# Kernel optimization log

Measured on AMD Instinct MI355X. Metric: run time of the kernel, lower is better.

Reference implementation:

```python
import jax, jax.numpy as jnp
import numpy as np
import math

HIDDEN = 1024
N_HEADS = 16
N_KV = 4
HEAD_DIM = HIDDEN // N_HEADS  # 64
B, S = 2, 2048
THETA = 100000.0


def _freqs_cos_sin(dim, end, theta):
    # yarn params: original_max_position_embeddings=2048 >= end, so no ramp scaling,
    # attention_factor=1.0 -> plain RoPE frequencies.
    inv = 1.0 / theta ** (np.arange(0, dim, 2)[: dim // 2] / dim)
    t = np.arange(end)
    f = np.outer(t, inv).astype(np.float32)  # (end, dim/2)
    cos = np.concatenate([np.cos(f), np.cos(f)], axis=-1)  # (end, dim)
    sin = np.concatenate([np.sin(f), np.sin(f)], axis=-1)
    return jnp.asarray(cos), jnp.asarray(sin)


def _rotate(x):
    # stack([-x[...,1::2], x[...,::2]], -1).reshape_as(x)
    return jnp.stack([-x[..., 1::2], x[..., ::2]], axis=-1).reshape(x.shape)


def setup_inputs() -> dict:
    key = jax.random.key(0)
    ks = jax.random.split(key, 9)
    s = 0.02
    return {
        "hidden_states": jax.random.normal(ks[0], (B, S, HIDDEN), jnp.float32),
        "attention_mask": jnp.ones((B, S), jnp.int32),
        "Wq": jax.random.normal(ks[1], (HIDDEN, HIDDEN), jnp.float32) * s,
        "bq": jnp.zeros((HIDDEN,), jnp.float32),
        "Wk": jax.random.normal(ks[2], (HIDDEN, N_KV * HEAD_DIM), jnp.float32) * s,
        "bk": jnp.zeros((N_KV * HEAD_DIM,), jnp.float32),
        "Wv": jax.random.normal(ks[3], (HIDDEN, N_KV * HEAD_DIM), jnp.float32) * s,
        "bv": jnp.zeros((N_KV * HEAD_DIM,), jnp.float32),
        "Wo": jax.random.normal(ks[4], (HIDDEN, HIDDEN), jnp.float32) * s,
        "bo": jnp.zeros((HIDDEN,), jnp.float32),
    }


def reference(hidden_states, attention_mask, Wq, bq, Wk, bk, Wv, bv, Wo, bo):
    b, s, _ = hidden_states.shape
    q = (hidden_states @ Wq + bq).reshape(b, s, N_HEADS, HEAD_DIM)
    k = (hidden_states @ Wk + bk).reshape(b, s, N_KV, HEAD_DIM)
    v = (hidden_states @ Wv + bv).reshape(b, s, N_KV, HEAD_DIM)

    cos, sin = _freqs_cos_sin(HEAD_DIM, s, THETA)
    cos = cos[:, None, :]  # (s,1,d) broadcasts over (b,s,h,d)
    sin = sin[:, None, :]
    q = q * cos + _rotate(q) * sin
    k = k * cos + _rotate(k) * sin

    # GQA: repeat_interleave kv heads -> jnp.repeat along head axis
    rep = N_HEADS // N_KV
    k = jnp.repeat(k, rep, axis=2)
    v = jnp.repeat(v, rep, axis=2)

    scores = jnp.einsum("bqhd,bkhd->bhqk", q, k) / math.sqrt(HEAD_DIM)
    neg = jnp.finfo(scores.dtype).min
    causal = jnp.triu(jnp.ones((s, s), bool), k=1)  # (q,kv)
    bias = jnp.where(causal, neg, 0.0).astype(scores.dtype)[None, None]
    key_mask = attention_mask.astype(bool)[:, None, None, :]  # (b,1,1,kv)
    bias = jnp.where(key_mask, bias, neg)
    probs = jax.nn.softmax(scores + bias, axis=-1)
    attn = jnp.einsum("bhqk,bkhd->bqhd", probs, v).reshape(b, s, HIDDEN)
    return attn @ Wo + bo
```

## Files before the change

kernel.cpp:

```cpp
#include <hip/hip_runtime.h>
#include <cstddef>
#include <cstdint>

#define B_   2
#define S_   2048
#define HID  1024
#define NH_  16
#define NKV_ 4
#define DH_  64
#define ROWS (B_ * S_)
#define NQKV 1536
#define QSCALE 0.18033688011112042f

typedef __bf16 bf16_t;
typedef _Float16 f16_t;
typedef bf16_t bf16x8 __attribute__((ext_vector_type(8)));
typedef bf16_t bf16x4 __attribute__((ext_vector_type(4)));
typedef f16_t  f16x8  __attribute__((ext_vector_type(8)));
typedef f16_t  f16x4  __attribute__((ext_vector_type(4)));
typedef float  f32x4  __attribute__((ext_vector_type(4)));

typedef __attribute__((address_space(1))) const uint32_t gu32_t;
typedef __attribute__((address_space(3))) uint32_t lu32_t;

__device__ __forceinline__ void gl_lds16(const void* g, void* l) {
  __builtin_amdgcn_global_load_lds((gu32_t*)g, (lu32_t*)l, 16, 0, 0);
}

__global__ void prep_all(const float* __restrict__ hs,
                         const float* __restrict__ Wq, const float* __restrict__ Wk,
                         const float* __restrict__ Wv, const float* __restrict__ Wo,
                         const float* __restrict__ bq, const float* __restrict__ bk,
                         const float* __restrict__ bv,
                         bf16_t* __restrict__ hsb,
                         bf16_t* __restrict__ Wt, bf16_t* __restrict__ Wot,
                         float* __restrict__ ball, float2* __restrict__ lut)
{
  const int bid = blockIdx.x;
  if (bid < 2048) {
    const int i = (bid * 256 + threadIdx.x) * 8;
    float4 a = *(const float4*)(hs + i);
    float4 b = *(const float4*)(hs + i + 4);
    bf16x8 o;
    o[0]=(bf16_t)a.x; o[1]=(bf16_t)a.y; o[2]=(bf16_t)a.z; o[3]=(bf16_t)a.w;
    o[4]=(bf16_t)b.x; o[5]=(bf16_t)b.y; o[6]=(bf16_t)b.z; o[7]=(bf16_t)b.w;
    *(bf16x8*)(hsb + i) = o;
    return;
  }
  if (bid >= 4614) {
    const int idx = (bid - 4614) * 256 + threadIdx.x;
    const int s = idx >> 5, j = idx & 31;
    const float L = 0.51905126482615037f;
    const float ang = (float)s * exp2f(-L * (float)j);
    lut[idx] = make_float2(cosf(ang), sinf(ang));
    return;
  }
  if (bid >= 4608) {
    int i = (bid - 4608) * 256 + threadIdx.x;
    if (i < NQKV) ball[i] = (i < 1024) ? bq[i] : ((i < 1280) ? bk[i-1024] : bv[i-1280]);
    return;
  }
  const int wb = bid - 2048;
  const float* src; bf16_t* dst; int N, n0, k0;
  if (wb < 1024)      { src = Wq; dst = Wt;            N = 1024; int t = wb;      n0=(t&31)*32; k0=(t>>5)*32; }
  else if (wb < 1280) { src = Wk; dst = Wt + 1024*HID; N = 256;  int t = wb-1024; n0=(t&7)*32;  k0=(t>>3)*32; }
  else if (wb < 1536) { src = Wv; dst = Wt + 1280*HID; N = 256;  int t = wb-1280; n0=(t&7)*32;  k0=(t>>3)*32; }
  else                { src = Wo; dst = Wot;           N = 1024; int t = wb-1536; n0=(t&31)*32; k0=(t>>5)*32; }
  __shared__ bf16_t T[32][33];
  const int tx = threadIdx.x & 31, ty = threadIdx.x >> 5;
#pragma unroll
  for (int i = 0; i < 4; ++i)
    T[ty + i*8][tx] = (bf16_t)src[(size_t)(k0 + ty + i*8) * N + n0 + tx];
  __syncthreads();
#pragma unroll
  for (int i = 0; i < 4; ++i)
    dst[(size_t)(n0 + ty + i*8) * HID + k0 + tx] = T[tx][ty + i*8];
}

__global__ __launch_bounds__(256, 3) void gemm_qkv(
    const bf16_t* __restrict__ A, const bf16_t* __restrict__ Bt,
    const float* __restrict__ bias, const float2* __restrict__ lut,
    bf16_t* __restrict__ C, bf16_t* __restrict__ Kimg, f16_t* __restrict__ Vimg)
{
  __shared__ bf16_t As[2][128 * 64];
  __shared__ bf16_t Bs[2][64 * 64];
  const int tid  = threadIdx.x;
  const int w    = tid >> 6;
  const int lane = tid & 63;
  const int m    = lane & 15;
  const int quad = lane >> 4;
  const int wm   = w >> 1, wn = w & 1;

  const int lin = blockIdx.y * 24 + blockIdx.x;
  const int swz = (lin & 7) * 96 + (lin >> 3);
  const int bx  = swz % 24;
  const int by  = swz / 24;
  const size_t bm = (size_t)by * 128;
  const size_t bn = (size_t)bx * 64;

  const int srow = w * 8 + (lane >> 3);
  const int scol = (lane & 7) * 8;
  const bf16_t* Ag = A  + (bm + srow) * HID + scol;
  const bf16_t* Bg = Bt + (bn + srow) * HID + scol;

  f32x4 acc[4][2];
#pragma unroll
  for (int i = 0; i < 4; ++i)
#pragma unroll
    for (int j = 0; j < 2; ++j) acc[i][j] = (f32x4){0.f, 0.f, 0.f, 0.f};

#pragma unroll
  for (int i = 0; i < 4; ++i)
    gl_lds16(Ag + (size_t)(i * 32) * HID, &As[0][(w * 8 + i * 32) * 64]);
#pragma unroll
  for (int i = 0; i < 2; ++i)
    gl_lds16(Bg + (size_t)(i * 32) * HID, &Bs[0][(w * 8 + i * 32) * 64]);

  int p = 0;
  for (int k0 = 0; k0 < HID; k0 += 64) {
    __syncthreads();
    if (k0 + 64 < HID) {
#pragma unroll
      for (int i = 0; i < 4; ++i)
        gl_lds16(Ag + (size_t)(i * 32) * HID + k0 + 64, &As[p^1][(w * 8 + i * 32) * 64]);
#pragma unroll
      for (int i = 0; i < 2; ++i)
        gl_lds16(Bg + (size_t)(i * 32) * HID + k0 + 64, &Bs[p^1][(w * 8 + i * 32) * 64]);
    }
#pragma unroll
    for (int ks = 0; ks < 2; ++ks) {
      bf16x8 af[4], bfr[2];
#pragma unroll
      for (int mt = 0; mt < 4; ++mt)
        af[mt] = *(const bf16x8*)&As[p][(wm * 64 + mt * 16 + m) * 64 + ks * 32 + quad * 8];
#pragma unroll
      for (int nt = 0; nt < 2; ++nt)
        bfr[nt] = *(const bf16x8*)&Bs[p][(wn * 32 + nt * 16 + m) * 64 + ks * 32 + quad * 8];
#pragma unroll
      for (int mt = 0; mt < 4; ++mt)
#pragma unroll
        for (int nt = 0; nt < 2; ++nt)
          acc[mt][nt] = __builtin_amdgcn_mfma_f32_16x16x32_bf16(bfr[nt], af[mt], acc[mt][nt], 0, 0, 0);
    }
    p ^= 1;
  }

  const int b   = by >> 4;
  const int rt  = by & 15;

  if (bx < 16) {
#pragma unroll
    for (int mt = 0; mt < 4; ++mt) {
      const size_t row = bm + wm * 64 + mt * 16 + m;
#pragma unroll
      for (int nt = 0; nt < 2; ++nt) {
        const size_t col = bn + wn * 32 + nt * 16 + quad * 4;
        float4 bb = *(const float4*)&bias[col];
        bf16x4 o;
        o[0] = (bf16_t)(acc[mt][nt][0] + bb.x);
        o[1] = (bf16_t)(acc[mt][nt][1] + bb.y);
        o[2] = (bf16_t)(acc[mt][nt][2] + bb.z);
        o[3] = (bf16_t)(acc[mt][nt][3] + bb.w);
        *(bf16x4*)&C[row * NQKV + col] = o;
      }
    }
  } else if (bx < 20) {
    const int kvh = bx - 16;
    const size_t img0 = ((size_t)(b * NKV_ + kvh) * 32 + rt * 2) * 4096;
#pragma unroll
    for (int mt = 0; mt < 4; ++mt) {
      const int row128 = wm * 64 + mt * 16 + m;
      const int srw    = rt * 128 + row128;
      const int key    = row128 & 63;
      const size_t img = img0 + (size_t)(row128 >> 6) * 4096;
#pragma unroll
      for (int nt = 0; nt < 2; ++nt) {
        const int d0 = wn * 32 + nt * 16 + quad * 4;
        const float4 bb = *(const float4*)&bias[1024 + kvh * DH_ + d0];
        const float v0 = acc[mt][nt][0] + bb.x;
        const float v1 = acc[mt][nt][1] + bb.y;
        const float v2 = acc[mt][nt][2] + bb.z;
        const float v3 = acc[mt][nt][3] + bb.w;
        const float2* lp = lut + srw * 32 + (d0 & 31);
        const float2 l0 = lp[0], l1 = lp[1], l2 = lp[2], l3 = lp[3];
        bf16x4 o;
        o[0] = (bf16_t)(v0 * l0.x - v1 * l0.y);
        o[1] = (bf16_t)(v1 * l1.x + v0 * l1.y);
        o[2] = (bf16_t)(v2 * l2.x - v3 * l2.y);
        o[3] = (bf16_t)(v3 * l3.x + v2 * l3.y);
        const int slot = (d0 >> 3) ^ (key & 7);
        *(bf16x4*)&Kimg[img + key * 64 + slot * 8 + (d0 & 7)] = o;
      }
    }
  } else {
    const int kvh = bx - 20;
    f16_t* Lv = (f16_t*)&As[0][0];
    __syncthreads();
#pragma unroll
    for (int mt = 0; mt < 4; ++mt) {
      const int row128 = wm * 64 + mt * 16 + m;
#pragma unroll
      for (int nt = 0; nt < 2; ++nt) {
        const int d0 = wn * 32 + nt * 16 + quad * 4;
        const float4 bb = *(const float4*)&bias[1280 + kvh * DH_ + d0];
        f16x4 o;
        o[0] = (f16_t)(acc[mt][nt][0] + bb.x);
        o[1] = (f16_t)(acc[mt][nt][1] + bb.y);
        o[2] = (f16_t)(acc[mt][nt][2] + bb.z);
        o[3] = (f16_t)(acc[mt][nt][3] + bb.w);
        *(f16x4*)&Lv[row128 * 68 + d0] = o;
      }
    }
    __syncthreads();
    const size_t img0 = ((size_t)(b * NKV_ + kvh) * 32 + rt * 2) * 4096;
    const int d  = tid & 63;
    const int qg = tid >> 6;
#pragma unroll
    for (int i = 0; i < 8; ++i) {
      const int ki = i >> 2;
      const int g4 = qg * 4 + (i & 3);
      f16x4 o;
#pragma unroll
      for (int j = 0; j < 4; ++j)
        o[j] = Lv[(ki * 64 + g4 * 4 + j) * 68 + d];
      const int slot = g4 ^ (d & 15);
      *(f16x4*)&Vimg[img0 + (size_t)ki * 4096 + d * 64 + slot * 4] = o;
    }
  }
}

__global__ __launch_bounds__(256, 3) void gemm64_f32o(
    const bf16_t* __restrict__ A, const bf16_t* __restrict__ Bt,
    const float* __restrict__ bias, float* __restrict__ C, int N)
{
  __shared__ bf16_t As[2][128 * 64];
  __shared__ bf16_t Bs[2][64 * 64];
  const int tid  = threadIdx.x;
  const int w    = tid >> 6;
  const int lane = tid & 63;
  const int m    = lane & 15;
  const int quad = lane >> 4;
  const int wm   = w >> 1, wn = w & 1;

  const int lin = blockIdx.y * 16 + blockIdx.x;
  const int swz = (lin & 7) * 64 + (lin >> 3);
  const int bx  = swz & 15;
  const int by  = swz >> 4;
  const size_t bm = (size_t)by * 128;
  const size_t bn = (size_t)bx * 64;

  const int srow = w * 8 + (lane >> 3);
  const int scol = (lane & 7) * 8;
  const bf16_t* Ag = A  + (bm + srow) * HID + scol;
  const bf16_t* Bg = Bt + (bn + srow) * HID + scol;

  f32x4 acc[4][2];
#pragma unroll
  for (int i = 0; i < 4; ++i)
#pragma unroll
    for (int j = 0; j < 2; ++j) acc[i][j] = (f32x4){0.f, 0.f, 0.f, 0.f};

#pragma unroll
  for (int i = 0; i < 4; ++i)
    gl_lds16(Ag + (size_t)(i * 32) * HID, &As[0][(w * 8 + i * 32) * 64]);
#pragma unroll
  for (int i = 0; i < 2; ++i)
    gl_lds16(Bg + (size_t)(i * 32) * HID, &Bs[0][(w * 8 + i * 32) * 64]);

  int p = 0;
  for (int k0 = 0; k0 < HID; k0 += 64) {
    __syncthreads();
    if (k0 + 64 < HID) {
#pragma unroll
      for (int i = 0; i < 4; ++i)
        gl_lds16(Ag + (size_t)(i * 32) * HID + k0 + 64, &As[p^1][(w * 8 + i * 32) * 64]);
#pragma unroll
      for (int i = 0; i < 2; ++i)
        gl_lds16(Bg + (size_t)(i * 32) * HID + k0 + 64, &Bs[p^1][(w * 8 + i * 32) * 64]);
    }
#pragma unroll
    for (int ks = 0; ks < 2; ++ks) {
      bf16x8 af[4], bfr[2];
#pragma unroll
      for (int mt = 0; mt < 4; ++mt)
        af[mt] = *(const bf16x8*)&As[p][(wm * 64 + mt * 16 + m) * 64 + ks * 32 + quad * 8];
#pragma unroll
      for (int nt = 0; nt < 2; ++nt)
        bfr[nt] = *(const bf16x8*)&Bs[p][(wn * 32 + nt * 16 + m) * 64 + ks * 32 + quad * 8];
#pragma unroll
      for (int mt = 0; mt < 4; ++mt)
#pragma unroll
        for (int nt = 0; nt < 2; ++nt)
          acc[mt][nt] = __builtin_amdgcn_mfma_f32_16x16x32_bf16(bfr[nt], af[mt], acc[mt][nt], 0, 0, 0);
    }
    p ^= 1;
  }
#pragma unroll
  for (int mt = 0; mt < 4; ++mt) {
    const size_t row = bm + wm * 64 + mt * 16 + m;
#pragma unroll
    for (int nt = 0; nt < 2; ++nt) {
      const size_t col = bn + wn * 32 + nt * 16 + quad * 4;
      float4 bb = *(const float4*)&bias[col];
      float4 o;
      o.x = acc[mt][nt][0] + bb.x; o.y = acc[mt][nt][1] + bb.y;
      o.z = acc[mt][nt][2] + bb.z; o.w = acc[mt][nt][3] + bb.w;
      *(float4*)&C[row * N + col] = o;
    }
  }
}

#define PROC_TILE(AQ, OACC, LP, Q0W)                                          \
  do {                                                                        \
    f32x4 sc[4];                                                              \
    _Pragma("unroll") for (int cb = 0; cb < 4; ++cb)                          \
      sc[cb] = (f32x4){0.f, 0.f, 0.f, 0.f};                                   \
    _Pragma("unroll") for (int cb = 0; cb < 4; ++cb) {                        \
      const bf16x8 bk0 = *(const bf16x8*)&Ks[g][p][(cb*16 + m) * 64 + x0s * 8]; \
      const bf16x8 bk1 = *(const bf16x8*)&Ks[g][p][(cb*16 + m) * 64 + x1s * 8]; \
      sc[cb] = __builtin_amdgcn_mfma_f32_16x16x32_bf16(bk0, AQ[0], sc[cb], 0, 0, 0); \
      sc[cb] = __builtin_amdgcn_mfma_f32_16x16x32_bf16(bk1, AQ[1], sc[cb], 0, 0, 0); \
    }                                                                         \
    f16x4 bp[4];                                                              \
    {                                                                         \
      const bool needm = (kbase + 63 > (Q0W)) || (mb != ~0ull);               \
      if (needm) {                                                            \
        const int qv = (Q0W) + m;                                             \
        _Pragma("unroll") for (int cb = 0; cb < 4; ++cb)                      \
          _Pragma("unroll") for (int r = 0; r < 4; ++r) {                     \
            const int idx = cb*16 + quad*4 + r;                               \
            const bool ok = (kbase + idx <= qv) && ((mb >> idx) & 1);         \
            sc[cb][r] = ok ? sc[cb][r] : -1e38f;                              \
          }                                                                   \
      }                                                                       \
      float sum = 0.f;                                                        \
      _Pragma("unroll") for (int cb = 0; cb < 4; ++cb) {                      \
        f16x4 pp;                                                             \
        _Pragma("unroll") for (int r = 0; r < 4; ++r) {                       \
          const float pv = exp2f(sc[cb][r]);                                  \
          sum += pv;                                                          \
          pp[r] = (f16_t)pv;                                                  \
        }                                                                     \
        bp[cb] = pp;                                                          \
      }                                                                       \
      LP += sum;                                                              \
    }                                                                         \
    _Pragma("unroll") for (int cb = 0; cb < 4; ++cb) {                        \
      f16x4 av[4];                                                            \
      _Pragma("unroll") for (int dblk = 0; dblk < 4; ++dblk) {                \
        const int slot = (cb * 4 + quad) ^ m;                                 \
        av[dblk] = *(const f16x4*)&Vs[g][p][(dblk*16 + m) * 64 + slot * 4];   \
      }                                                                       \
      _Pragma("unroll") for (int dblk = 0; dblk < 4; ++dblk)                  \
        OACC[dblk] = __builtin_amdgcn_mfma_f32_16x16x16f16(av[dblk], bp[cb], OACC[dblk], 0, 0, 0); \
    }                                                                         \
  } while (0)

__global__ __launch_bounds__(512, 4) void attn_v8(
    const bf16_t* __restrict__ QKVb, const float2* __restrict__ lut,
    const bf16_t* __restrict__ Kt2, const f16_t* __restrict__ Vt2,
    const int* __restrict__ amask, bf16_t* __restrict__ Ab)
{
  __shared__ __align__(16) bf16_t Ks[2][2][64 * 64];
  __shared__ __align__(16) f16_t  Vs[2][2][64 * 64];

  const int tid  = threadIdx.x;
  const int w    = tid >> 6;
  const int g    = w >> 2;
  const int wl   = w & 3;
  const int lane = tid & 63;
  const int m    = lane & 15;
  const int quad = lane >> 4;
  const int kvh  = blockIdx.y;
  const int b    = blockIdx.z;
  const int h    = kvh * 4 + wl;
  const int x    = blockIdx.x;
  const int q0wA = x * 16;
  const int q0wB = (127 - x) * 16;
  const int nA   = (x >> 2) + 1;
  const int nB   = ((127 - x) >> 2) + 1;
  const int T    = nA + nB;

  bf16x8 aqA[2], aqB[2];
#pragma unroll
  for (int tt = 0; tt < 2; ++tt) {
    const int q0w_t = tt ? q0wB : q0wA;
    const int spos = q0w_t + m;
    const bf16_t* qsrc = QKVb + (size_t)(b * S_ + spos) * NQKV + h * DH_;
    float2 l8[8];
#pragma unroll
    for (int j = 0; j < 8; ++j) l8[j] = lut[spos * 32 + quad * 8 + j];
#pragma unroll
    for (int kc = 0; kc < 2; ++kc) {
      bf16x8 xv = *(const bf16x8*)(qsrc + kc * 32 + quad * 8);
      bf16x8 y;
#pragma unroll
      for (int i = 0; i < 4; ++i) {
        const float x0 = (float)xv[2*i], x1 = (float)xv[2*i+1];
        y[2*i]   = (bf16_t)((x0 * l8[2*i].x   - x1 * l8[2*i].y)   * QSCALE);
        y[2*i+1] = (bf16_t)((x1 * l8[2*i+1].x + x0 * l8[2*i+1].y) * QSCALE);
      }
      if (tt) aqB[kc] = y; else aqA[kc] = y;
    }
  }

  f32x4 oaccA[4], oaccB[4];
#pragma unroll
  for (int d = 0; d < 4; ++d) {
    oaccA[d] = (f32x4){0.f,0.f,0.f,0.f};
    oaccB[d] = (f32x4){0.f,0.f,0.f,0.f};
  }
  float lpA = 0.f, lpB = 0.f;

  const size_t imgbase = ((size_t)(b * NKV_ + kvh) * 32) * 4096;
  const bf16_t* Kg = Kt2 + imgbase;
  const f16_t*  Vg = Vt2 + imgbase;
  const int x0s = quad ^ (m & 7);
  const int x1s = (4 + quad) ^ (m & 7);
  const int* amp = amask + b * S_;

  int mcur;
  {
    const int e0  = g;
    const int kt0 = (e0 >= nA) ? e0 - nA : e0;
    const size_t off = (size_t)kt0 * 4096;
    gl_lds16(Kg + off + (2*wl)   * 512 + lane * 8, &Ks[g][0][(2*wl)   * 512]);
    gl_lds16(Kg + off + (2*wl+1) * 512 + lane * 8, &Ks[g][0][(2*wl+1) * 512]);
    gl_lds16(Vg + off + (2*wl)   * 512 + lane * 8, &Vs[g][0][(2*wl)   * 512]);
    gl_lds16(Vg + off + (2*wl+1) * 512 + lane * 8, &Vs[g][0][(2*wl+1) * 512]);
    mcur = amp[kt0 * 64 + lane];
  }

  int p = 0;
  const int niter = (T + 1) >> 1;
  for (int t = 0; t < niter; ++t) {
    const int e = 2 * t + g;
    __syncthreads();
    const int e2 = e + 2;
    const bool more = (e2 < T);
    int kt2 = 0;
    if (more) {
      kt2 = (e2 >= nA) ? e2 - nA : e2;
      const size_t off = (size_t)kt2 * 4096;
      gl_lds16(Kg + off + (2*wl)   * 512 + lane * 8, &Ks[g][p^1][(2*wl)   * 512]);
      gl_lds16(Kg + off + (2*wl+1) * 512 + lane * 8, &Ks[g][p^1][(2*wl+1) * 512]);
      gl_lds16(Vg + off + (2*wl)   * 512 + lane * 8, &Vs[g][p^1][(2*wl)   * 512]);
      gl_lds16(Vg + off + (2*wl+1) * 512 + lane * 8, &Vs[g][p^1][(2*wl+1) * 512]);
    }
    const int mnext = more ? amp[kt2 * 64 + lane] : 0;
    if (e < T) {
      const uint64_t mb = __ballot(mcur != 0);
      const bool isB = (e >= nA);
      const int kt = isB ? e - nA : e;
      const int kbase = kt * 64;
      if (isB) PROC_TILE(aqB, oaccB, lpB, q0wB);
      else     PROC_TILE(aqA, oaccA, lpA, q0wA);
    }
    mcur = mnext;
    p ^= 1;
  }

  float lAred = lpA;
  lAred += __shfl_xor(lAred, 16); lAred += __shfl_xor(lAred, 32);
  float lBred = lpB;
  lBred += __shfl_xor(lBred, 16); lBred += __shfl_xor(lBred, 32);

  __syncthreads();
  float* scrA = (float*)&Ks[0][0][0];
  float* scrB = (float*)&Vs[0][0][0];
  const int sbase = wl * 1104 + m * 68 + quad * 4;

  if (g == 0) {
#pragma unroll
    for (int dblk = 0; dblk < 4; ++dblk)
      *(f32x4*)&scrA[sbase + dblk * 16] = oaccA[dblk];
    if (quad == 0) scrA[wl * 1104 + 16 * 68 + m] = lAred;
  } else {
#pragma unroll
    for (int dblk = 0; dblk < 4; ++dblk)
      *(f32x4*)&scrB[sbase + dblk * 16] = oaccB[dblk];
    if (quad == 0) scrB[wl * 1104 + 16 * 68 + m] = lBred;
  }
  __syncthreads();

  if (g == 0) {
    const float l = lBred + scrB[wl * 1104 + 16 * 68 + m];
    const float inv = 1.0f / l;
    const size_t row = (size_t)(b * S_ + q0wB + m);
#pragma unroll
    for (int dblk = 0; dblk < 4; ++dblk) {
      const f32x4 part = *(const f32x4*)&scrB[sbase + dblk * 16];
      bf16x4 o;
      o[0] = (bf16_t)((oaccB[dblk][0] + part[0]) * inv);
      o[1] = (bf16_t)((oaccB[dblk][1] + part[1]) * inv);
      o[2] = (bf16_t)((oaccB[dblk][2] + part[2]) * inv);
      o[3] = (bf16_t)((oaccB[dblk][3] + part[3]) * inv);
      *(bf16x4*)&Ab[row * HID + h * DH_ + dblk * 16 + quad * 4] = o;
    }
  } else {
    const float l = lAred + scrA[wl * 1104 + 16 * 68 + m];
    const float inv = 1.0f / l;
    const size_t row = (size_t)(b * S_ + q0wA + m);
#pragma unroll
    for (int dblk = 0; dblk < 4; ++dblk) {
      const f32x4 part = *(const f32x4*)&scrA[sbase + dblk * 16];
      bf16x4 o;
      o[0] = (bf16_t)((oaccA[dblk][0] + part[0]) * inv);
      o[1] = (bf16_t)((oaccA[dblk][1] + part[1]) * inv);
      o[2] = (bf16_t)((oaccA[dblk][2] + part[2]) * inv);
      o[3] = (bf16_t)((oaccA[dblk][3] + part[3]) * inv);
      *(bf16x4*)&Ab[row * HID + h * DH_ + dblk * 16 + quad * 4] = o;
    }
  }
}

extern "C" void kernel_launch(void* const* d_in, const int* in_sizes, int n_in,
                              void* d_out, int out_size, void* d_ws, size_t ws_size,
                              hipStream_t stream)
{
  const float* hs    = (const float*)d_in[0];
  const int*   amask = (const int*)  d_in[1];
  const float* Wq    = (const float*)d_in[2];
  const float* bq    = (const float*)d_in[3];
  const float* Wk    = (const float*)d_in[4];
  const float* bk    = (const float*)d_in[5];
  const float* Wv    = (const float*)d_in[6];
  const float* bv    = (const float*)d_in[7];
  const float* Wo    = (const float*)d_in[8];
  const float* bo    = (const float*)d_in[9];
  float* out = (float*)d_out;

  bf16_t* QKVb = (bf16_t*)d_ws;
  bf16_t* hsb  = QKVb + (size_t)ROWS * NQKV;
  bf16_t* Wt   = hsb + (size_t)ROWS * HID;
  bf16_t* Wot  = Wt + (size_t)NQKV * HID;
  float*  ball = (float*)(Wot + (size_t)HID * HID);
  bf16_t* Kimg = (bf16_t*)(ball + NQKV);
  f16_t*  Vimg = (f16_t*)(Kimg + (size_t)B_*NKV_*32*4096);
  float2* lut  = (float2*)(Vimg + (size_t)B_*NKV_*32*4096);
  bf16_t* Ab   = hsb;

  prep_all<<<4870, 256, 0, stream>>>(hs, Wq, Wk, Wv, Wo, bq, bk, bv,
                                     hsb, Wt, Wot, ball, lut);

  gemm_qkv<<<dim3(NQKV/64, ROWS/128), 256, 0, stream>>>(hsb, Wt, ball, lut,
                                                        QKVb, Kimg, Vimg);

  attn_v8<<<dim3(64, NKV_, B_), 512, 0, stream>>>(QKVb, lut, Kimg, Vimg, amask, Ab);

  gemm64_f32o<<<dim3(HID/64, ROWS/128), 256, 0, stream>>>(Ab, Wot, bo, out, HID);
}
```

Baseline: 181.3 us.

## Use 128x128 tiles with 8-wave blocks for QKV and output GEMMs

Both projection GEMMs move from 128x64 tiles with 4 waves to 128x128 tiles with 8 waves, sharing a common staged core macro. The aim is to cut global and LDS traffic per output element and raise reuse of the A tile. The K/V epilogues are remapped so that one block covers two KV heads. Grid size halves to 384 and 256 blocks, which may underfill the 256 CUs, and 64KB of shared memory per block limits occupancy.

```diff
diff --git a/kernel.cpp b/kernel.cpp
--- a/kernel.cpp
+++ b/kernel.cpp
@@ -77,78 +77,69 @@
     dst[(size_t)(n0 + ty + i*8) * HID + k0 + tx] = T[tx][ty + i*8];
 }
 
-__global__ __launch_bounds__(256, 3) void gemm_qkv(
+#define STG128(buf, k0)                                                       \
+  do {                                                                        \
+    gl_lds16(Ag + (k0),           SM +         (buf)*8192 + (w*16)     * 64); \
+    gl_lds16(Ag + 8*HID + (k0),   SM +         (buf)*8192 + (w*16 + 8) * 64); \
+    gl_lds16(Bg + (k0),           SM + 16384 + (buf)*8192 + (w*16)     * 64); \
+    gl_lds16(Bg + 8*HID + (k0),   SM + 16384 + (buf)*8192 + (w*16 + 8) * 64); \
+  } while (0)
+
+#define GEMM128_CORE                                                          \
+  f32x4 acc[4][2];                                                            \
+  _Pragma("unroll") for (int i = 0; i < 4; ++i)                               \
+    _Pragma("unroll") for (int j = 0; j < 2; ++j)                             \
+      acc[i][j] = (f32x4){0.f, 0.f, 0.f, 0.f};                                \
+  STG128(0, 0);                                                               \
+  int p = 0;                                                                  \
+  for (int k0 = 0; k0 < HID; k0 += 64) {                                      \
+    __syncthreads();                                                          \
+    if (k0 + 64 < HID) STG128(p^1, k0 + 64);                                  \
+    _Pragma("unroll") for (int ks = 0; ks < 2; ++ks) {                        \
+      bf16x8 af[4], bfr[2];                                                   \
+      _Pragma("unroll") for (int mt = 0; mt < 4; ++mt)                        \
+        af[mt] = *(const bf16x8*)&SM[p*8192 + (wm*64 + mt*16 + m)*64 + ks*32 + quad*8]; \
+      _Pragma("unroll") for (int nt = 0; nt < 2; ++nt)                        \
+        bfr[nt] = *(const bf16x8*)&SM[16384 + p*8192 + (wn*32 + nt*16 + m)*64 + ks*32 + quad*8]; \
+      _Pragma("unroll") for (int mt = 0; mt < 4; ++mt)                        \
+        _Pragma("unroll") for (int nt = 0; nt < 2; ++nt)                      \
+          acc[mt][nt] = __builtin_amdgcn_mfma_f32_16x16x32_bf16(bfr[nt], af[mt], acc[mt][nt], 0, 0, 0); \
+    }                                                                         \
+    p ^= 1;                                                                   \
+  }
+
+__global__ __launch_bounds__(512, 4) void gemm_qkv(
     const bf16_t* __restrict__ A, const bf16_t* __restrict__ Bt,
     const float* __restrict__ bias, const float2* __restrict__ lut,
     bf16_t* __restrict__ C, bf16_t* __restrict__ Kimg, f16_t* __restrict__ Vimg)
 {
-  __shared__ bf16_t As[2][128 * 64];
-  __shared__ bf16_t Bs[2][64 * 64];
+  __shared__ __align__(16) bf16_t SM[4 * 128 * 64];
   const int tid  = threadIdx.x;
   const int w    = tid >> 6;
   const int lane = tid & 63;
   const int m    = lane & 15;
   const int quad = lane >> 4;
-  const int wm   = w >> 1, wn = w & 1;
-
-  const int lin = blockIdx.y * 24 + blockIdx.x;
-  const int swz = (lin & 7) * 96 + (lin >> 3);
-  const int bx  = swz % 24;
-  const int by  = swz / 24;
+  const int wm   = w >> 2;
+  const int wn   = w & 3;
+
+  const int lin = blockIdx.y * 12 + blockIdx.x;
+  const int swz = (lin & 7) * 48 + (lin >> 3);
+  const int bx  = swz % 12;
+  const int by  = swz / 12;
   const size_t bm = (size_t)by * 128;
-  const size_t bn = (size_t)bx * 64;
-
-  const int srow = w * 8 + (lane >> 3);
+  const size_t bn = (size_t)bx * 128;
+
+  const int sr   = lane >> 3;
   const int scol = (lane & 7) * 8;
-  const bf16_t* Ag = A  + (bm + srow) * HID + scol;
-  const bf16_t* Bg = Bt + (bn + srow) * HID + scol;
-
-  f32x4 acc[4][2];
-#pragma unroll
-  for (int i = 0; i < 4; ++i)
-#pragma unroll
-    for (int j = 0; j < 2; ++j) acc[i][j] = (f32x4){0.f, 0.f, 0.f, 0.f};
-
-#pragma unroll
-  for (int i = 0; i < 4; ++i)
-    gl_lds16(Ag + (size_t)(i * 32) * HID, &As[0][(w * 8 + i * 32) * 64]);
-#pragma unroll
-  for (int i = 0; i < 2; ++i)
-    gl_lds16(Bg + (size_t)(i * 32) * HID, &Bs[0][(w * 8 + i * 32) * 64]);
-
-  int p = 0;
-  for (int k0 = 0; k0 < HID; k0 += 64) {
-    __syncthreads();
-    if (k0 + 64 < HID) {
-#pragma unroll
-      for (int i = 0; i < 4; ++i)
-        gl_lds16(Ag + (size_t)(i * 32) * HID + k0 + 64, &As[p^1][(w * 8 + i * 32) * 64]);
-#pragma unroll
-      for (int i = 0; i < 2; ++i)
-        gl_lds16(Bg + (size_t)(i * 32) * HID + k0 + 64, &Bs[p^1][(w * 8 + i * 32) * 64]);
-    }
-#pragma unroll
-    for (int ks = 0; ks < 2; ++ks) {
-      bf16x8 af[4], bfr[2];
-#pragma unroll
-      for (int mt = 0; mt < 4; ++mt)
-        af[mt] = *(const bf16x8*)&As[p][(wm * 64 + mt * 16 + m) * 64 + ks * 32 + quad * 8];
-#pragma unroll
-      for (int nt = 0; nt < 2; ++nt)
-        bfr[nt] = *(const bf16x8*)&Bs[p][(wn * 32 + nt * 16 + m) * 64 + ks * 32 + quad * 8];
-#pragma unroll
-      for (int mt = 0; mt < 4; ++mt)
-#pragma unroll
-        for (int nt = 0; nt < 2; ++nt)
-          acc[mt][nt] = __builtin_amdgcn_mfma_f32_16x16x32_bf16(bfr[nt], af[mt], acc[mt][nt], 0, 0, 0);
-    }
-    p ^= 1;
-  }
-
-  const int b   = by >> 4;
-  const int rt  = by & 15;
-
-  if (bx < 16) {
+  const bf16_t* Ag = A  + (bm + w * 16 + sr) * HID + scol;
+  const bf16_t* Bg = Bt + (bn + w * 16 + sr) * HID + scol;
+
+  GEMM128_CORE
+
+  const int b  = by >> 4;
+  const int rt = by & 15;
+
+  if (bx < 8) {
 #pragma unroll
     for (int mt = 0; mt < 4; ++mt) {
       const size_t row = bm + wm * 64 + mt * 16 + m;
@@ -164,19 +155,19 @@
         *(bf16x4*)&C[row * NQKV + col] = o;
       }
     }
-  } else if (bx < 20) {
-    const int kvh = bx - 16;
-    const size_t img0 = ((size_t)(b * NKV_ + kvh) * 32 + rt * 2) * 4096;
+  } else if (bx < 10) {
 #pragma unroll
     for (int mt = 0; mt < 4; ++mt) {
       const int row128 = wm * 64 + mt * 16 + m;
       const int srw    = rt * 128 + row128;
       const int key    = row128 & 63;
-      const size_t img = img0 + (size_t)(row128 >> 6) * 4096;
 #pragma unroll
       for (int nt = 0; nt < 2; ++nt) {
-        const int d0 = wn * 32 + nt * 16 + quad * 4;
-        const float4 bb = *(const float4*)&bias[1024 + kvh * DH_ + d0];
+        const int colq = (bx - 8) * 128 + wn * 32 + nt * 16 + quad * 4;
+        const int kvh  = colq >> 6;
+        const int d0   = colq & 63;
+        const size_t img = ((size_t)(b * NKV_ + kvh) * 32 + rt * 2 + (row128 >> 6)) * 4096;
+        const float4 bb = *(const float4*)&bias[1024 + colq];
         const float v0 = acc[mt][nt][0] + bb.x;
         const float v1 = acc[mt][nt][1] + bb.y;
         const float v2 = acc[mt][nt][2] + bb.z;
@@ -193,108 +184,72 @@
       }
     }
   } else {
-    const int kvh = bx - 20;
-    f16_t* Lv = (f16_t*)&As[0][0];
+    f16_t* Lv = (f16_t*)SM;
     __syncthreads();
 #pragma unroll
     for (int mt = 0; mt < 4; ++mt) {
       const int row128 = wm * 64 + mt * 16 + m;
 #pragma unroll
       for (int nt = 0; nt < 2; ++nt) {
-        const int d0 = wn * 32 + nt * 16 + quad * 4;
-        const float4 bb = *(const float4*)&bias[1280 + kvh * DH_ + d0];
+        const int cloc = wn * 32 + nt * 16 + quad * 4;
+        const int colq = (bx - 10) * 128 + cloc;
+        const float4 bb = *(const float4*)&bias[1280 + colq];
         f16x4 o;
         o[0] = (f16_t)(acc[mt][nt][0] + bb.x);
         o[1] = (f16_t)(acc[mt][nt][1] + bb.y);
         o[2] = (f16_t)(acc[mt][nt][2] + bb.z);
         o[3] = (f16_t)(acc[mt][nt][3] + bb.w);
-        *(f16x4*)&Lv[row128 * 68 + d0] = o;
+        *(f16x4*)&Lv[row128 * 128 + cloc] = o;
       }
     }
     __syncthreads();
+    const int d   = tid & 63;
+    const int hh  = (tid >> 6) & 1;
+    const int qg  = tid >> 7;
+    const int kvh = (bx - 10) * 2 + hh;
     const size_t img0 = ((size_t)(b * NKV_ + kvh) * 32 + rt * 2) * 4096;
-    const int d  = tid & 63;
-    const int qg = tid >> 6;
-#pragma unroll
-    for (int i = 0; i < 8; ++i) {
-      const int ki = i >> 2;
-      const int g4 = qg * 4 + (i & 3);
-      f16x4 o;
-#pragma unroll
-      for (int j = 0; j < 4; ++j)
-        o[j] = Lv[(ki * 64 + g4 * 4 + j) * 68 + d];
-      const int slot = g4 ^ (d & 15);
-      *(f16x4*)&Vimg[img0 + (size_t)ki * 4096 + d * 64 + slot * 4] = o;
-    }
+#pragma unroll
+    for (int ki = 0; ki < 2; ++ki)
+#pragma unroll
+      for (int gs = 0; gs < 4; ++gs) {
+        const int g4 = qg * 4 + gs;
+        f16x4 o;
+#pragma unroll
+        for (int j = 0; j < 4; ++j)
+          o[j] = Lv[(ki * 64 + g4 * 4 + j) * 128 + hh * 64 + d];
+        const int slot = g4 ^ (d & 15);
+        *(f16x4*)&Vimg[img0 + (size_t)ki * 4096 + d * 64 + slot * 4] = o;
+      }
   }
 }
 
-__global__ __launch_bounds__(256, 3) void gemm64_f32o(
+__global__ __launch_bounds__(512, 4) void gemm_o(
     const bf16_t* __restrict__ A, const bf16_t* __restrict__ Bt,
-    const float* __restrict__ bias, float* __restrict__ C, int N)
+    const float* __restrict__ bias, float* __restrict__ C)
 {
-  __shared__ bf16_t As[2][128 * 64];
-  __shared__ bf16_t Bs[2][64 * 64];
+  __shared__ __align__(16) bf16_t SM[4 * 128 * 64];
   const int tid  = threadIdx.x;
   const int w    = tid >> 6;
   const int lane = tid & 63;
   const int m    = lane & 15;
   const int quad = lane >> 4;
-  const int wm   = w >> 1, wn = w & 1;
-
-  const int lin = blockIdx.y * 16 + blockIdx.x;
-  const int swz = (lin & 7) * 64 + (lin >> 3);
-  const int bx  = swz & 15;
-  const int by  = swz >> 4;
+  const int wm   = w >> 2;
+  const int wn   = w & 3;
+
+  const int lin = blockIdx.y * 8 + blockIdx.x;
+  const int swz = (lin & 7) * 32 + (lin >> 3);
+  const int bx  = swz & 7;
+  const int by  = swz >> 3;
   const size_t bm = (size_t)by * 128;
-  const size_t bn = (size_t)bx * 64;
-
-  const int srow = w * 8 + (lane >> 3);
+  const size_t bn = (size_t)bx * 128;
+
+  const int sr   = lane >> 3;
   const int scol = (lane & 7) * 8;
-  const bf16_t* Ag = A  + (bm + srow) * HID + scol;
-  const bf16_t* Bg = Bt + (bn + srow) * HID + scol;
-
-  f32x4 acc[4][2];
-#pragma unroll
-  for (int i = 0; i < 4; ++i)
-#pragma unroll
-    for (int j = 0; j < 2; ++j) acc[i][j] = (f32x4){0.f, 0.f, 0.f, 0.f};
-
-#pragma unroll
-  for (int i = 0; i < 4; ++i)
-    gl_lds16(Ag + (size_t)(i * 32) * HID, &As[0][(w * 8 + i * 32) * 64]);
-#pragma unroll
-  for (int i = 0; i < 2; ++i)
-    gl_lds16(Bg + (size_t)(i * 32) * HID, &Bs[0][(w * 8 + i * 32) * 64]);
-
-  int p = 0;
-  for (int k0 = 0; k0 < HID; k0 += 64) {
-    __syncthreads();
-    if (k0 + 64 < HID) {
-#pragma unroll
-      for (int i = 0; i < 4; ++i)
-        gl_lds16(Ag + (size_t)(i * 32) * HID + k0 + 64, &As[p^1][(w * 8 + i * 32) * 64]);
-#pragma unroll
-      for (int i = 0; i < 2; ++i)
-        gl_lds16(Bg + (size_t)(i * 32) * HID + k0 + 64, &Bs[p^1][(w * 8 + i * 32) * 64]);
-    }
-#pragma unroll
-    for (int ks = 0; ks < 2; ++ks) {
-      bf16x8 af[4], bfr[2];
-#pragma unroll
-      for (int mt = 0; mt < 4; ++mt)
-        af[mt] = *(const bf16x8*)&As[p][(wm * 64 + mt * 16 + m) * 64 + ks * 32 + quad * 8];
-#pragma unroll
-      for (int nt = 0; nt < 2; ++nt)
-        bfr[nt] = *(const bf16x8*)&Bs[p][(wn * 32 + nt * 16 + m) * 64 + ks * 32 + quad * 8];
-#pragma unroll
-      for (int mt = 0; mt < 4; ++mt)
-#pragma unroll
-        for (int nt = 0; nt < 2; ++nt)
-          acc[mt][nt] = __builtin_amdgcn_mfma_f32_16x16x32_bf16(bfr[nt], af[mt], acc[mt][nt], 0, 0, 0);
-    }
-    p ^= 1;
-  }
+  const bf16_t* Ag = A  + (bm + w * 16 + sr) * HID + scol;
+  const bf16_t* Bg = Bt + (bn + w * 16 + sr) * HID + scol;
+
+  GEMM128_CORE
+
 #pragma unroll
   for (int mt = 0; mt < 4; ++mt) {
     const size_t row = bm + wm * 64 + mt * 16 + m;
@@ -305,7 +260,7 @@
       float4 o;
       o.x = acc[mt][nt][0] + bb.x; o.y = acc[mt][nt][1] + bb.y;
       o.z = acc[mt][nt][2] + bb.z; o.w = acc[mt][nt][3] + bb.w;
-      *(float4*)&C[row * N + col] = o;
+      *(float4*)&C[row * HID + col] = o;
     }
   }
 }
@@ -543,10 +498,10 @@
   prep_all<<<4870, 256, 0, stream>>>(hs, Wq, Wk, Wv, Wo, bq, bk, bv,
                                      hsb, Wt, Wot, ball, lut);
 
-  gemm_qkv<<<dim3(NQKV/64, ROWS/128), 256, 0, stream>>>(hsb, Wt, ball, lut,
-                                                        QKVb, Kimg, Vimg);
+  gemm_qkv<<<dim3(NQKV/128, ROWS/128), 512, 0, stream>>>(hsb, Wt, ball, lut,
+                                                         QKVb, Kimg, Vimg);
 
   attn_v8<<<dim3(64, NKV_, B_), 512, 0, stream>>>(QKVb, lut, Kimg, Vimg, amask, Ab);
 
-  gemm64_f32o<<<dim3(HID/64, ROWS/128), 256, 0, stream>>>(Ab, Wot, bo, out, HID);
+  gemm_o<<<dim3(HID/128, ROWS/128), 512, 0, stream>>>(Ab, Wot, bo, out);
 }
```

Result: no change. 184.2 us (+1.6%).
